# Optimization experiments

Hardware: AMD Instinct MI355X
Metric: run time of the kernel (lower is better)

## Reference

```python
import jax, jax.numpy as jnp
import numpy as np

B, D = 4096, 768

def setup_inputs() -> dict:
    key = jax.random.key(0)
    k1, k2 = jax.random.split(key)
    embeddings = jax.random.normal(k1, (B, D), dtype=jnp.float32)
    # precomputed articulatory distance matrix (stand-in for articulatory_distance_fn over word pairs)
    art_dist = jax.random.uniform(k2, (B, B), dtype=jnp.float32)
    return {"embeddings": embeddings, "art_dist": art_dist}

def reference(embeddings, art_dist):
    b = embeddings.shape[0]
    # pairwise squared L2 distances via Gram matrix: ||ei||^2 + ||ej||^2 - 2 ei.ej
    sq = jnp.sum(embeddings * embeddings, axis=1)                  # [B]
    gram = jnp.einsum('id,jd->ij', embeddings, embeddings)         # [B, B]
    d2 = sq[:, None] + sq[None, :] - 2.0 * gram                    # [B, B]
    off_diag = 1.0 - jnp.eye(b, dtype=embeddings.dtype)            # exclude i == j
    pair_loss = (d2 - art_dist) ** 2
    pairs_count = b * (b - 1)
    return jnp.sum(pair_loss * off_diag) / pairs_count
```

## Files before the change

kernel.cpp:

```cpp
#include <hip/hip_runtime.h>
#include <hip/hip_bf16.h>

#define B_DIM 4096
#define D_DIM 768
#define BM 256
#define BK 64
#define NSTEP (D_DIM / BK)
#define NTI (B_DIM / BM)

typedef __bf16 bf16_t;
typedef bf16_t bf16x8 __attribute__((ext_vector_type(8)));
typedef float f32x4 __attribute__((ext_vector_type(4)));

static __device__ __forceinline__ ushort f2bf(float v) {
    __hip_bfloat16 h = __float2bfloat16(v);
    return *reinterpret_cast<const ushort*>(&h);
}

__global__ __launch_bounds__(256) void prep_kernel(
    const float* __restrict__ E, ushort* __restrict__ Ebf, float* __restrict__ sq)
{
    const int lane = threadIdx.x & 63;
    const int row  = blockIdx.x * 4 + (threadIdx.x >> 6);
    const float4* er = reinterpret_cast<const float4*>(E + (size_t)row * D_DIM);
    ushort4* br = reinterpret_cast<ushort4*>(Ebf + (size_t)row * D_DIM);
    float s = 0.f;
    #pragma unroll
    for (int k = 0; k < 3; ++k) {
        float4 v = er[lane + 64 * k];
        s += v.x * v.x + v.y * v.y + v.z * v.z + v.w * v.w;
        ushort4 o;
        o.x = f2bf(v.x); o.y = f2bf(v.y); o.z = f2bf(v.z); o.w = f2bf(v.w);
        br[lane + 64 * k] = o;
    }
    #pragma unroll
    for (int off = 32; off > 0; off >>= 1) s += __shfl_down(s, off);
    if (lane == 0) sq[row] = s;
}

__device__ __forceinline__ void stage_step(
    const ushort* __restrict__ Ebf, ushort* Adst, ushort* Bdst,
    int row0, int col0, int kk, int tid)
{
    #pragma unroll
    for (int q = 0; q < 4; ++q) {
        const int idx = q * 512 + tid;
        const int rl  = idx >> 3;
        const int c16 = idx & 7;
        const int cg  = (c16 ^ (rl & 7)) << 3;
        const ushort* gA = Ebf + (size_t)(row0 + rl) * D_DIM + kk + cg;
        __builtin_amdgcn_global_load_lds(
            (const __attribute__((address_space(1))) void*)gA,
            (__attribute__((address_space(3))) void*)(Adst + rl * 64 + c16 * 8),
            16, 0, 0);
        const ushort* gB = Ebf + (size_t)(col0 + rl) * D_DIM + kk + cg;
        __builtin_amdgcn_global_load_lds(
            (const __attribute__((address_space(1))) void*)gB,
            (__attribute__((address_space(3))) void*)(Bdst + rl * 64 + c16 * 8),
            16, 0, 0);
    }
}

__device__ __forceinline__ void compute_step(
    const ushort* Acur, const ushort* Bcur, f32x4 (&acc)[8][4],
    int wr, int wc, int lane)
{
    const int l15 = lane & 15;
    const int kq  = (lane >> 4) * 8;
    bf16x8 bv[4][2];
    #pragma unroll
    for (int nn = 0; nn < 4; ++nn)
        #pragma unroll
        for (int k2 = 0; k2 < 2; ++k2) {
            const int rb = wc * 64 + nn * 16 + l15;
            const int c  = (k2 * 32 + kq) ^ ((rb & 7) << 3);
            bv[nn][k2] = *reinterpret_cast<const bf16x8*>(Bcur + rb * 64 + c);
        }
    #pragma unroll
    for (int mm = 0; mm < 8; ++mm) {
        const int ra = wr * 128 + mm * 16 + l15;
        const bf16x8 af0 = *reinterpret_cast<const bf16x8*>(
            Acur + ra * 64 + (kq ^ ((ra & 7) << 3)));
        const bf16x8 af1 = *reinterpret_cast<const bf16x8*>(
            Acur + ra * 64 + ((32 + kq) ^ ((ra & 7) << 3)));
        __builtin_amdgcn_s_setprio(1);
        #pragma unroll
        for (int nn = 0; nn < 4; ++nn) {
            acc[mm][nn] = __builtin_amdgcn_mfma_f32_16x16x32_bf16(
                af0, bv[nn][0], acc[mm][nn], 0, 0, 0);
            acc[mm][nn] = __builtin_amdgcn_mfma_f32_16x16x32_bf16(
                af1, bv[nn][1], acc[mm][nn], 0, 0, 0);
        }
        __builtin_amdgcn_s_setprio(0);
    }
}

__global__ __launch_bounds__(512, 2) void gram_loss_kernel(
    const ushort* __restrict__ Ebf, const float* __restrict__ sq,
    const float* __restrict__ art, float* __restrict__ out)
{
    extern __shared__ char smem[];
    ushort* Ab = (ushort*)smem;
    ushort* Bb = (ushort*)(smem + 49152);
    float*  red = (float*)(smem + 98304);

    const int tid  = threadIdx.x;
    const int lane = tid & 63;
    const int wave = tid >> 6;
    const int wr = wave >> 2;
    const int wc = wave & 3;

    const int swz = (blockIdx.x & 7) * 32 + (blockIdx.x >> 3);
    const int tileR = swz >> 4;
    const int tileC = swz & 15;
    const int row0 = tileR * BM;
    const int col0 = tileC * BM;

    f32x4 acc[8][4] = {};

    stage_step(Ebf, Ab, Bb, row0, col0, 0, tid);
    stage_step(Ebf, Ab + 8192, Bb + 8192, row0, col0, BK, tid);

    #pragma unroll 3
    for (int st = 0; st < NSTEP; ++st) {
        const int cur = st % 3;
        const int pre = (st + 2) % 3;
        const int kpre = ((st + 2) % NSTEP) * BK;

        asm volatile("s_waitcnt vmcnt(8)" ::: "memory");
        __builtin_amdgcn_s_barrier();
        __builtin_amdgcn_sched_barrier(0);

        stage_step(Ebf, Ab + pre * 8192, Bb + pre * 8192, row0, col0, kpre, tid);
        compute_step(Ab + cur * 8192, Bb + cur * 8192, acc, wr, wc, lane);
    }

    float lsum = 0.f;
    const int lr = (lane >> 4) * 4;
    const int lc = lane & 15;
    const int rbase = row0 + wr * 128;
    const int cbase = col0 + wc * 64;

    if (tileR != tileC) {
        #pragma unroll
        for (int m = 0; m < 8; ++m) {
            const int gi0 = rbase + m * 16 + lr;
            const float4 sqv = *reinterpret_cast<const float4*>(sq + gi0);
            const float sqi[4] = { sqv.x, sqv.y, sqv.z, sqv.w };
            #pragma unroll
            for (int n = 0; n < 4; ++n) {
                const int gj = cbase + n * 16 + lc;
                const float sqj = sq[gj];
                const float4 am = *reinterpret_cast<const float4*>(
                    &art[(size_t)gj * B_DIM + gi0]);
                const float amv[4] = { am.x, am.y, am.z, am.w };
                #pragma unroll
                for (int j = 0; j < 4; ++j) {
                    const float d2 = sqi[j] + sqj - 2.0f * acc[m][n][j];
                    const float t = d2 - amv[j];
                    lsum += t * t;
                }
            }
        }
    } else {
        #pragma unroll
        for (int m = 0; m < 8; ++m) {
            const int gi0 = rbase + m * 16 + lr;
            const float4 sqv = *reinterpret_cast<const float4*>(sq + gi0);
            const float sqi[4] = { sqv.x, sqv.y, sqv.z, sqv.w };
            #pragma unroll
            for (int n = 0; n < 4; ++n) {
                const int gj = cbase + n * 16 + lc;
                const float sqj = sq[gj];
                const float4 am = *reinterpret_cast<const float4*>(
                    &art[(size_t)gj * B_DIM + gi0]);
                const float amv[4] = { am.x, am.y, am.z, am.w };
                #pragma unroll
                for (int j = 0; j < 4; ++j) {
                    const int gi = gi0 + j;
                    const float d2 = sqi[j] + sqj - 2.0f * acc[m][n][j];
                    const float t = d2 - amv[j];
                    if (gi != gj) lsum += t * t;
                }
            }
        }
    }

    #pragma unroll
    for (int off = 32; off > 0; off >>= 1) lsum += __shfl_down(lsum, off);
    if (lane == 0) red[wave] = lsum;
    __syncthreads();
    if (tid == 0) {
        float tot = 0.f;
        #pragma unroll
        for (int w = 0; w < 8; ++w) tot += red[w];
        const float inv_pairs = 1.0f / ((float)B_DIM * (float)(B_DIM - 1));
        atomicAdd(out, tot * inv_pairs);
    }
}

extern "C" void kernel_launch(void* const* d_in, const int* in_sizes, int n_in,
                              void* d_out, int out_size, void* d_ws, size_t ws_size,
                              hipStream_t stream) {
    const float* E   = (const float*)d_in[0];
    const float* art = (const float*)d_in[1];
    float* out = (float*)d_out;

    ushort* Ebf = (ushort*)d_ws;
    float*  sq  = (float*)((char*)d_ws + (size_t)B_DIM * D_DIM * 2);

    const int lds_bytes = 98304 + 64;
    (void)hipFuncSetAttribute((const void*)gram_loss_kernel,
                              hipFuncAttributeMaxDynamicSharedMemorySize, lds_bytes);

    hipMemsetAsync(d_out, 0, sizeof(float), stream);
    prep_kernel<<<B_DIM / 4, 256, 0, stream>>>(E, Ebf, sq);
    gram_loss_kernel<<<NTI * NTI, 512, lds_bytes, stream>>>(Ebf, sq, art, out);
}
```

Before: 128.3 us.

## Split each K-step into four phases interleaving LDS reads, prefetch and MFMA

The main loop now splits each K-step into four quadrant phases. In each phase the kernel reads a subset of A/B fragments from LDS, issues one quarter of the next-stage global-to-LDS prefetch, then runs a block of MFMAs between workgroup barriers. The aim is to interleave memory issue with matrix math and cut register pressure from holding all B fragments, in the style of ping-pong scheduling. The trade is four extra barriers per K-step plus lgkmcnt waits, which could serialise the waves.

```diff
diff --git a/kernel.cpp b/kernel.cpp
--- a/kernel.cpp
+++ b/kernel.cpp
@@ -38,61 +38,77 @@
     if (lane == 0) sq[row] = s;
 }
 
-__device__ __forceinline__ void stage_step(
+template<int SQ>
+__device__ __forceinline__ void stage_quarter(
     const ushort* __restrict__ Ebf, ushort* Adst, ushort* Bdst,
     int row0, int col0, int kk, int tid)
 {
-    #pragma unroll
-    for (int q = 0; q < 4; ++q) {
+    const ushort* gbase = (SQ < 2) ? (Ebf + (size_t)row0 * D_DIM)
+                                   : (Ebf + (size_t)col0 * D_DIM);
+    ushort* lbase = (SQ < 2) ? Adst : Bdst;
+    const int rbase = (SQ & 1) * 128;
+    #pragma unroll
+    for (int q = 0; q < 2; ++q) {
         const int idx = q * 512 + tid;
-        const int rl  = idx >> 3;
+        const int rl  = rbase + (idx >> 3);
         const int c16 = idx & 7;
         const int cg  = (c16 ^ (rl & 7)) << 3;
-        const ushort* gA = Ebf + (size_t)(row0 + rl) * D_DIM + kk + cg;
+        const ushort* g = gbase + (size_t)rl * D_DIM + kk + cg;
         __builtin_amdgcn_global_load_lds(
-            (const __attribute__((address_space(1))) void*)gA,
-            (__attribute__((address_space(3))) void*)(Adst + rl * 64 + c16 * 8),
+            (const __attribute__((address_space(1))) void*)g,
+            (__attribute__((address_space(3))) void*)(lbase + rl * 64 + c16 * 8),
             16, 0, 0);
-        const ushort* gB = Ebf + (size_t)(col0 + rl) * D_DIM + kk + cg;
-        __builtin_amdgcn_global_load_lds(
-            (const __attribute__((address_space(1))) void*)gB,
-            (__attribute__((address_space(3))) void*)(Bdst + rl * 64 + c16 * 8),
-            16, 0, 0);
-    }
-}
-
-__device__ __forceinline__ void compute_step(
-    const ushort* Acur, const ushort* Bcur, f32x4 (&acc)[8][4],
-    int wr, int wc, int lane)
+    }
+}
+
+template<int QM, int QN, bool READB, int SQ>
+__device__ __forceinline__ void do_phase(
+    const ushort* Acur, const ushort* Bcur,
+    const ushort* __restrict__ Ebf, ushort* Adst, ushort* Bdst,
+    int row0, int col0, int kpre,
+    f32x4 (&acc)[8][4], bf16x8 (&bv)[2][2], int wr, int wc, int lane, int tid)
 {
     const int l15 = lane & 15;
     const int kq  = (lane >> 4) * 8;
-    bf16x8 bv[4][2];
-    #pragma unroll
-    for (int nn = 0; nn < 4; ++nn)
+
+    if (READB) {
+        #pragma unroll
+        for (int nn = 0; nn < 2; ++nn)
+            #pragma unroll
+            for (int k2 = 0; k2 < 2; ++k2) {
+                const int rb = wc * 64 + (QN * 2 + nn) * 16 + l15;
+                const int c  = (k2 * 32 + kq) ^ ((rb & 7) << 3);
+                bv[nn][k2] = *reinterpret_cast<const bf16x8*>(Bcur + rb * 64 + c);
+            }
+    }
+    bf16x8 af[4][2];
+    #pragma unroll
+    for (int mm = 0; mm < 4; ++mm)
         #pragma unroll
         for (int k2 = 0; k2 < 2; ++k2) {
-            const int rb = wc * 64 + nn * 16 + l15;
-            const int c  = (k2 * 32 + kq) ^ ((rb & 7) << 3);
-            bv[nn][k2] = *reinterpret_cast<const bf16x8*>(Bcur + rb * 64 + c);
+            const int ra = wr * 128 + (QM * 4 + mm) * 16 + l15;
+            const int c  = (k2 * 32 + kq) ^ ((ra & 7) << 3);
+            af[mm][k2] = *reinterpret_cast<const bf16x8*>(Acur + ra * 64 + c);
         }
-    #pragma unroll
-    for (int mm = 0; mm < 8; ++mm) {
-        const int ra = wr * 128 + mm * 16 + l15;
-        const bf16x8 af0 = *reinterpret_cast<const bf16x8*>(
-            Acur + ra * 64 + (kq ^ ((ra & 7) << 3)));
-        const bf16x8 af1 = *reinterpret_cast<const bf16x8*>(
-            Acur + ra * 64 + ((32 + kq) ^ ((ra & 7) << 3)));
-        __builtin_amdgcn_s_setprio(1);
-        #pragma unroll
-        for (int nn = 0; nn < 4; ++nn) {
-            acc[mm][nn] = __builtin_amdgcn_mfma_f32_16x16x32_bf16(
-                af0, bv[nn][0], acc[mm][nn], 0, 0, 0);
-            acc[mm][nn] = __builtin_amdgcn_mfma_f32_16x16x32_bf16(
-                af1, bv[nn][1], acc[mm][nn], 0, 0, 0);
-        }
-        __builtin_amdgcn_s_setprio(0);
-    }
+
+    stage_quarter<SQ>(Ebf, Adst, Bdst, row0, col0, kpre, tid);
+
+    __builtin_amdgcn_sched_barrier(0);
+    __builtin_amdgcn_s_barrier();
+    asm volatile("s_waitcnt lgkmcnt(0)" ::: "memory");
+    __builtin_amdgcn_sched_barrier(0);
+    __builtin_amdgcn_s_setprio(1);
+    #pragma unroll
+    for (int mm = 0; mm < 4; ++mm)
+        #pragma unroll
+        for (int nn = 0; nn < 2; ++nn)
+            #pragma unroll
+            for (int k2 = 0; k2 < 2; ++k2)
+                acc[QM * 4 + mm][QN * 2 + nn] = __builtin_amdgcn_mfma_f32_16x16x32_bf16(
+                    af[mm][k2], bv[nn][k2], acc[QM * 4 + mm][QN * 2 + nn], 0, 0, 0);
+    __builtin_amdgcn_s_setprio(0);
+    __builtin_amdgcn_sched_barrier(0);
+    __builtin_amdgcn_s_barrier();
 }
 
 __global__ __launch_bounds__(512, 2) void gram_loss_kernel(
@@ -118,21 +134,38 @@
 
     f32x4 acc[8][4] = {};
 
-    stage_step(Ebf, Ab, Bb, row0, col0, 0, tid);
-    stage_step(Ebf, Ab + 8192, Bb + 8192, row0, col0, BK, tid);
+    stage_quarter<0>(Ebf, Ab, Bb, row0, col0, 0, tid);
+    stage_quarter<1>(Ebf, Ab, Bb, row0, col0, 0, tid);
+    stage_quarter<2>(Ebf, Ab, Bb, row0, col0, 0, tid);
+    stage_quarter<3>(Ebf, Ab, Bb, row0, col0, 0, tid);
+    stage_quarter<0>(Ebf, Ab + 8192, Bb + 8192, row0, col0, BK, tid);
+    stage_quarter<1>(Ebf, Ab + 8192, Bb + 8192, row0, col0, BK, tid);
+    stage_quarter<2>(Ebf, Ab + 8192, Bb + 8192, row0, col0, BK, tid);
+    stage_quarter<3>(Ebf, Ab + 8192, Bb + 8192, row0, col0, BK, tid);
 
     #pragma unroll 3
     for (int st = 0; st < NSTEP; ++st) {
         const int cur = st % 3;
         const int pre = (st + 2) % 3;
         const int kpre = ((st + 2) % NSTEP) * BK;
+        const ushort* Acur = Ab + cur * 8192;
+        const ushort* Bcur = Bb + cur * 8192;
+        ushort* Adst = Ab + pre * 8192;
+        ushort* Bdst = Bb + pre * 8192;
 
         asm volatile("s_waitcnt vmcnt(8)" ::: "memory");
         __builtin_amdgcn_s_barrier();
         __builtin_amdgcn_sched_barrier(0);
 
-        stage_step(Ebf, Ab + pre * 8192, Bb + pre * 8192, row0, col0, kpre, tid);
-        compute_step(Ab + cur * 8192, Bb + cur * 8192, acc, wr, wc, lane);
+        bf16x8 bv[2][2];
+        do_phase<0, 0, true,  0>(Acur, Bcur, Ebf, Adst, Bdst, row0, col0, kpre,
+                                 acc, bv, wr, wc, lane, tid);
+        do_phase<1, 0, false, 1>(Acur, Bcur, Ebf, Adst, Bdst, row0, col0, kpre,
+                                 acc, bv, wr, wc, lane, tid);
+        do_phase<0, 1, true,  2>(Acur, Bcur, Ebf, Adst, Bdst, row0, col0, kpre,
+                                 acc, bv, wr, wc, lane, tid);
+        do_phase<1, 1, false, 3>(Acur, Bcur, Ebf, Adst, Bdst, row0, col0, kpre,
+                                 acc, bv, wr, wc, lane, tid);
     }
 
     float lsum = 0.f;
```

Measured after the change: 128.9 us. Within noise of the previous version (+0.5%).
